# Optimization experiments

Hardware: AMD Instinct MI355X
Metric: run time of the kernel (lower is better)

The kernel has to match this reference:

```python
import jax, jax.numpy as jnp
import numpy as np

EPS = 1e-6
NUM_HEADS = 16


def _layernorm(x, g, b):
    m = jnp.mean(x, axis=-1, keepdims=True)
    v = jnp.mean(jnp.square(x - m), axis=-1, keepdims=True)
    return (x - m) / jnp.sqrt(v + EPS) * g + b


def _rotate_half(x):
    x1, x2 = jnp.split(x, 2, axis=-1)
    return jnp.concatenate([-x2, x1], axis=-1)


def setup_inputs() -> dict:
    key = jax.random.key(0)
    B, N, C = 2, 2048, 1024
    H = NUM_HEADS
    D = C // H
    F = int(C * 4.0)
    ks = jax.random.split(key, 12)
    s = 0.02
    pos = jnp.arange(N)[:, None].astype(jnp.float32)
    inv_freq = 1.0 / (10000.0 ** (jnp.arange(0, D, 2, dtype=jnp.float32) / D))
    freqs = pos * inv_freq[None, :]          # [N, D/2]
    emb = jnp.concatenate([freqs, freqs], axis=-1)  # [N, D]
    return {
        "x": jax.random.normal(ks[0], (B, N, C), jnp.float32),
        "rotary_cos": jnp.cos(emb),
        "rotary_sin": jnp.sin(emb),
        "ln1_g": jnp.ones((C,), jnp.float32),
        "ln1_b": jnp.zeros((C,), jnp.float32),
        "Wq": jax.random.normal(ks[1], (C, C), jnp.float32) * s,
        "bq": jnp.zeros((C,), jnp.float32),
        "Wk": jax.random.normal(ks[2], (C, C), jnp.float32) * s,
        "bk": jnp.zeros((C,), jnp.float32),
        "Wv": jax.random.normal(ks[3], (C, C), jnp.float32) * s,
        "bv": jnp.zeros((C,), jnp.float32),
        "Wo": jax.random.normal(ks[4], (C, C), jnp.float32) * s,
        "bo": jnp.zeros((C,), jnp.float32),
        "ln2_g": jnp.ones((C,), jnp.float32),
        "ln2_b": jnp.zeros((C,), jnp.float32),
        "W1": jax.random.normal(ks[5], (F, C), jnp.float32) * s,
        "b1": jnp.zeros((F,), jnp.float32),
        "W2": jax.random.normal(ks[6], (C, F), jnp.float32) * s,
        "b2": jnp.zeros((C,), jnp.float32),
    }


def reference(x, rotary_cos, rotary_sin, ln1_g, ln1_b, Wq, bq, Wk, bk, Wv, bv,
              Wo, bo, ln2_g, ln2_b, W1, b1, W2, b2):
    B, N, C = x.shape
    H = NUM_HEADS
    D = C // H

    # --- attention branch ---
    h = _layernorm(x, ln1_g, ln1_b)
    q = (h @ Wq.T + bq).reshape(B, N, H, D).transpose(0, 2, 1, 3)  # [B,H,N,D]
    k = (h @ Wk.T + bk).reshape(B, N, H, D).transpose(0, 2, 1, 3)
    v = (h @ Wv.T + bv).reshape(B, N, H, D).transpose(0, 2, 1, 3)

    cos = rotary_cos[None, None, :, :]  # [1,1,N,D]
    sin = rotary_sin[None, None, :, :]
    q = q * cos + _rotate_half(q) * sin
    k = k * cos + _rotate_half(k) * sin

    scale = D ** -0.5
    attn = jnp.einsum('bhnd,bhmd->bhnm', q, k) * scale
    attn = jax.nn.softmax(attn, axis=-1)
    out = jnp.einsum('bhnm,bhmd->bhnd', attn, v)
    out = out.transpose(0, 2, 1, 3).reshape(B, N, C)
    out = out @ Wo.T + bo
    x = x + out

    # --- MLP branch ---
    h = _layernorm(x, ln2_g, ln2_b)
    h = jax.nn.gelu(h @ W1.T + b1, approximate=False)  # torch nn.GELU exact
    h = h @ W2.T + b2
    return x + h
```

## Files before the change

kernel.cpp:

```cpp
#include <hip/hip_runtime.h>
#include <hip/hip_bf16.h>

#define B_ 2
#define N_ 2048
#define C_ 1024
#define H_ 16
#define D_ 64
#define F_ 4096
#define M_ 4096

typedef __attribute__((ext_vector_type(8))) short bf16x8;
typedef __attribute__((ext_vector_type(4))) float f32x4;

__device__ inline unsigned short f2bf(float f) {
  unsigned int u = __float_as_uint(f);
  u = (u + 0x7FFFu + ((u >> 16) & 1u)) >> 16;
  return (unsigned short)u;
}
__device__ inline float bf2f(unsigned short u) {
  unsigned int x = ((unsigned int)u) << 16;
  return __uint_as_float(x);
}

__global__ __launch_bounds__(256)
void cvt_all(const float4* __restrict__ s0, const float4* __restrict__ s1,
             const float4* __restrict__ s2, const float4* __restrict__ s3,
             const float4* __restrict__ s4, const float4* __restrict__ s5,
             ushort4* __restrict__ d0, ushort4* __restrict__ d1,
             ushort4* __restrict__ d2, ushort4* __restrict__ d3,
             ushort4* __restrict__ d4, ushort4* __restrict__ d5) {
  int b = blockIdx.x;
  const float4* s; ushort4* d; int i;
  if      (b < 1024) { s = s0; d = d0; i = b * 256 + threadIdx.x; }
  else if (b < 2048) { s = s1; d = d1; i = (b - 1024) * 256 + threadIdx.x; }
  else if (b < 3072) { s = s2; d = d2; i = (b - 2048) * 256 + threadIdx.x; }
  else if (b < 4096) { s = s3; d = d3; i = (b - 3072) * 256 + threadIdx.x; }
  else if (b < 8192) { s = s4; d = d4; i = (b - 4096) * 256 + threadIdx.x; }
  else               { s = s5; d = d5; i = (b - 8192) * 256 + threadIdx.x; }
  float4 f = s[i];
  ushort4 o;
  o.x = f2bf(f.x); o.y = f2bf(f.y); o.z = f2bf(f.z); o.w = f2bf(f.w);
  d[i] = o;
}

__global__ __launch_bounds__(256)
void ln_kernel(const float* __restrict__ x, const float* __restrict__ g,
               const float* __restrict__ b, unsigned short* __restrict__ out) {
  __shared__ float red[8];
  const int row = blockIdx.x;
  const int t = threadIdx.x;
  const float4 xv = *(const float4*)(x + row * 1024 + t * 4);
  float s  = xv.x + xv.y + xv.z + xv.w;
  float sq = xv.x * xv.x + xv.y * xv.y + xv.z * xv.z + xv.w * xv.w;
  #pragma unroll
  for (int off = 32; off >= 1; off >>= 1) {
    s  += __shfl_down(s, off);
    sq += __shfl_down(sq, off);
  }
  const int lane = t & 63, wave = t >> 6;
  if (lane == 0) { red[wave * 2] = s; red[wave * 2 + 1] = sq; }
  __syncthreads();
  float ts = red[0] + red[2] + red[4] + red[6];
  float tq = red[1] + red[3] + red[5] + red[7];
  float mean = ts * (1.0f / 1024.0f);
  float var  = tq * (1.0f / 1024.0f) - mean * mean;
  float rstd = rsqrtf(var + 1e-6f);
  float xs[4] = {xv.x, xv.y, xv.z, xv.w};
  #pragma unroll
  for (int i = 0; i < 4; i++) {
    int c = t * 4 + i;
    float y = (xs[i] - mean) * rstd * g[c] + b[c];
    out[row * 1024 + c] = f2bf(y);
  }
}

template<int MODE, int BN>
__global__ __launch_bounds__(256)
void gemm_bt(const unsigned short* __restrict__ A,
             const unsigned short* __restrict__ Bw,
             int K, int Nout, int npc,
             const float* __restrict__ bias,
             const float* __restrict__ resid,
             unsigned short* __restrict__ out_bf,
             float* __restrict__ out_f32) {
  constexpr int NJ = BN / 32;
  static_assert(BN == 64, "vmcnt literal assumes 6 loads per stage");
  __shared__ unsigned short sA[3][128 * 64];
  __shared__ unsigned short sB[3][BN * 64];
  const int t = threadIdx.x;
  const int wave = t >> 6, lane = t & 63;
  const int quad = lane >> 4, l16 = lane & 15;
  const int wm = (wave & 1) * 64, wn = (wave >> 1) * (BN / 2);
  const int id = blockIdx.y * gridDim.x + blockIdx.x;
  const int xcd = id & 7, r_ = id >> 3;
  const int m_blk = xcd * 4 + (r_ & 3);
  const int n_blk = r_ >> 2;
  const int m0 = m_blk * 128, n0 = n_blk * BN;

  f32x4 acc[4][NJ];
  #pragma unroll
  for (int i = 0; i < 4; i++)
    #pragma unroll
    for (int j = 0; j < NJ; j++) acc[i][j] = (f32x4){0.f, 0.f, 0.f, 0.f};

  const int sc = (((t & 7) ^ ((t >> 3) & 7)) * 8);
  const unsigned short* gA = A  + (m0 + (t >> 3)) * K + sc;
  const unsigned short* gB = Bw + (n0 + (t >> 3)) * K + sc;

  auto stage = [&](int k0, int buf) {
    unsigned short* lA = &sA[buf][(wave * 8) * 64];
    unsigned short* lB = &sB[buf][(wave * 8) * 64];
    #pragma unroll
    for (int i = 0; i < 4; i++)
      __builtin_amdgcn_global_load_lds((const unsigned int*)(gA + (32 * i) * K + k0),
                                       (unsigned int*)(lA + 32 * i * 64), 16, 0, 0);
    #pragma unroll
    for (int i = 0; i < BN / 32; i++)
      __builtin_amdgcn_global_load_lds((const unsigned int*)(gB + (32 * i) * K + k0),
                                       (unsigned int*)(lB + 32 * i * 64), 16, 0, 0);
  };

  stage(0, 0);
  stage(64, 1);
  asm volatile("s_waitcnt vmcnt(6)" ::: "memory");
  __builtin_amdgcn_s_barrier();

  const int so0 = ((quad ^ (l16 & 7)) * 8);
  const int so1 = (((4 + quad) ^ (l16 & 7)) * 8);

  const int nk = K >> 6;
  int cur = 0;
  for (int kt = 0; kt < nk; kt++) {
    const unsigned short* rA = &sA[cur][0];
    const unsigned short* rB = &sB[cur][0];
    #pragma unroll
    for (int kk = 0; kk < 2; kk++) {
      const int so = kk ? so1 : so0;
      bf16x8 af[4], bfr[NJ];
      #pragma unroll
      for (int i = 0; i < 4; i++)
        af[i] = *(const bf16x8*)(&rA[(wm + i * 16 + l16) * 64 + so]);
      #pragma unroll
      for (int j = 0; j < NJ; j++)
        bfr[j] = *(const bf16x8*)(&rB[(wn + j * 16 + l16) * 64 + so]);
      #pragma unroll
      for (int i = 0; i < 4; i++)
        #pragma unroll
        for (int j = 0; j < NJ; j++)
          acc[i][j] = __builtin_amdgcn_mfma_f32_16x16x32_bf16(af[i], bfr[j], acc[i][j], 0, 0, 0);
    }
    if (kt + 2 < nk) {
      const int nb = (cur + 2 >= 3) ? cur - 1 : cur + 2;
      stage((kt + 2) * 64, nb);
      asm volatile("s_waitcnt vmcnt(6)" ::: "memory");
    } else {
      asm volatile("s_waitcnt vmcnt(0)" ::: "memory");
    }
    __builtin_amdgcn_s_barrier();
    cur = (cur == 2) ? 0 : cur + 1;
  }

  #pragma unroll
  for (int i = 0; i < 4; i++) {
    #pragma unroll
    for (int j = 0; j < NJ; j++) {
      int col = n0 + wn + j * 16 + l16;
      #pragma unroll
      for (int r = 0; r < 4; r++) {
        int row = m0 + wm + i * 16 + quad * 4 + r;
        float v = acc[i][j][r];
        if (MODE == 1 || MODE == 3) {
          out_f32[row * Nout + col] = v + bias[col] + resid[row * Nout + col];
        } else {
          v += bias[col];
          float w = v * (1.0f + 0.044715f * v * v);
          float gl = v / (1.0f + __expf(-1.5957691216f * w));
          out_bf[row * Nout + col] = f2bf(gl);
        }
      }
    }
  }
}

template<int EPI>
__global__ __launch_bounds__(512, 1)
void gemm256(const unsigned short* __restrict__ A,
             const unsigned short* __restrict__ Bw,
             const float* __restrict__ bias,
             const float* __restrict__ bq, const float* __restrict__ bk,
             const float* __restrict__ bv,
             const float* __restrict__ rc, const float* __restrict__ rs,
             unsigned short* __restrict__ o0,
             unsigned short* __restrict__ ko, unsigned short* __restrict__ vt) {
  const int K = 1024;
  __shared__ unsigned short sA[2][256 * 64];
  __shared__ unsigned short sB[2][256 * 64];
  const int t = threadIdx.x;
  const int wave = t >> 6, lane = t & 63;
  const int quad = lane >> 4, l16 = lane & 15;
  const int wm = (wave & 1) * 128, wn = (wave >> 1) * 64;
  const int id = blockIdx.x;
  const int xcd = id & 7, r_ = id >> 3;
  int m_blk, n_blk;
  if (EPI == 0) { n_blk = xcd * 2 + (r_ >> 4); m_blk = r_ & 15; }
  else          { m_blk = xcd * 2 + r_ / 12;   n_blk = r_ % 12; }
  const int m0 = m_blk * 256, n0 = n_blk * 256;

  f32x4 acc[8][4];
  #pragma unroll
  for (int i = 0; i < 8; i++)
    #pragma unroll
    for (int j = 0; j < 4; j++) acc[i][j] = (f32x4){0.f, 0.f, 0.f, 0.f};

  const int sc = (((t & 7) ^ ((t >> 3) & 7)) * 8);
  const unsigned short* gA = A  + (m0 + (t >> 3)) * K + sc;
  const unsigned short* gB = Bw + (n0 + (t >> 3)) * K + sc;

  auto stage_pair = [&](int k0, int buf, int pr) {
    if (pr < 2) {
      unsigned short* lA = &sA[buf][(wave * 8) * 64];
      #pragma unroll
      for (int r = pr * 2; r < pr * 2 + 2; r++)
        __builtin_amdgcn_global_load_lds((const unsigned int*)(gA + (64 * r) * K + k0),
                                         (unsigned int*)(lA + 64 * r * 64), 16, 0, 0);
    } else {
      unsigned short* lB = &sB[buf][(wave * 8) * 64];
      #pragma unroll
      for (int r = (pr - 2) * 2; r < (pr - 2) * 2 + 2; r++)
        __builtin_amdgcn_global_load_lds((const unsigned int*)(gB + (64 * r) * K + k0),
                                         (unsigned int*)(lB + 64 * r * 64), 16, 0, 0);
    }
  };

  stage_pair(0, 0, 0); stage_pair(0, 0, 1); stage_pair(0, 0, 2); stage_pair(0, 0, 3);
  stage_pair(64, 1, 0);
  asm volatile("s_waitcnt vmcnt(2)" ::: "memory");
  __builtin_amdgcn_s_barrier();

  const int so0 = ((quad ^ (l16 & 7)) * 8);
  const int so1 = (((4 + quad) ^ (l16 & 7)) * 8);

  const int nk = K >> 6;
  for (int t_ = 0; t_ < nk; t_++) {
    const int R = t_ & 1;
    const unsigned short* rA = sA[R];
    const unsigned short* rB = sB[R];
    #pragma unroll
    for (int kk = 0; kk < 2; kk++) {
      const int so = kk ? so1 : so0;
      bf16x8 af[8], bfr[4];
      #pragma unroll
      for (int ii = 0; ii < 8; ii++)
        af[ii] = *(const bf16x8*)(&rA[(wm + ii * 16 + l16) * 64 + so]);
      #pragma unroll
      for (int j = 0; j < 4; j++)
        bfr[j] = *(const bf16x8*)(&rB[(wn + j * 16 + l16) * 64 + so]);
      if (t_ + 1 < nk) {
        if (kk == 0) {
          stage_pair((t_ + 1) * 64, R ^ 1, 1);
        } else {
          stage_pair((t_ + 1) * 64, R ^ 1, 2);
          stage_pair((t_ + 1) * 64, R ^ 1, 3);
        }
      }
      __builtin_amdgcn_s_barrier();
      asm volatile("s_waitcnt lgkmcnt(0)" ::: "memory");
      __builtin_amdgcn_sched_barrier(0);
      __builtin_amdgcn_s_setprio(1);
      #pragma unroll
      for (int ii = 0; ii < 8; ii++)
        #pragma unroll
        for (int j = 0; j < 4; j++)
          acc[ii][j] =
              __builtin_amdgcn_mfma_f32_16x16x32_bf16(af[ii], bfr[j], acc[ii][j], 0, 0, 0);
      __builtin_amdgcn_s_setprio(0);
      if (kk == 0) __builtin_amdgcn_s_barrier();
    }
    __builtin_amdgcn_s_barrier();
    if (t_ + 2 < nk) {
      stage_pair((t_ + 2) * 64, R, 0);
      asm volatile("s_waitcnt vmcnt(2)" ::: "memory");
      __builtin_amdgcn_s_barrier();
    } else if (t_ + 1 < nk) {
      asm volatile("s_waitcnt vmcnt(0)" ::: "memory");
      __builtin_amdgcn_s_barrier();
    }
  }

  if (EPI == 0) {
    #pragma unroll
    for (int i = 0; i < 8; i++) {
      #pragma unroll
      for (int j = 0; j < 4; j++) {
        int col = n0 + wn + j * 16 + l16;
        float bb = bias[col];
        #pragma unroll
        for (int r = 0; r < 4; r++) {
          int row = m0 + wm + i * 16 + quad * 4 + r;
          float v = acc[i][j][r] + bb;
          float w = v * (1.0f + 0.044715f * v * v);
          float gl = v / (1.0f + __expf(-1.5957691216f * w));
          o0[row * 4096 + col] = f2bf(gl);
        }
      }
    }
  } else {
    const int rgn = n_blk >> 2;
    const int c0 = (n_blk & 3) * 256;
    if (rgn == 2) {
      #pragma unroll
      for (int i = 0; i < 8; i++) {
        int row0 = m0 + wm + i * 16 + quad * 4;
        int bidx = row0 >> 11, n0r = row0 & 2047;
        #pragma unroll
        for (int j = 0; j < 4; j++) {
          int d = j * 16 + l16;
          int c = c0 + wn + d;
          int h = c >> 6;
          float bb = bv[c];
          __hip_bfloat162 p01 = __float22bfloat162_rn(float2{acc[i][j][0] + bb, acc[i][j][1] + bb});
          __hip_bfloat162 p23 = __float22bfloat162_rn(float2{acc[i][j][2] + bb, acc[i][j][3] + bb});
          unsigned int u01, u23;
          __builtin_memcpy(&u01, &p01, 4);
          __builtin_memcpy(&u23, &p23, 4);
          *(uint2*)(vt + (((bidx * 16 + h) * 64) + d) * 2048 + n0r) = make_uint2(u01, u23);
        }
      }
    } else {
      const float* bia = (rgn == 0) ? bq : bk;
      unsigned short* outp = (rgn == 0) ? o0 : ko;
      #pragma unroll
      for (int i = 0; i < 8; i++) {
        #pragma unroll
        for (int r = 0; r < 4; r++) {
          int row = m0 + wm + i * 16 + quad * 4 + r;
          int bidx = row >> 11, n = row & 2047;
          #pragma unroll
          for (int j = 0; j < 4; j++) {
            int d = j * 16 + l16;
            int c = c0 + wn + d;
            int h = c >> 6;
            int oi = ((bidx * 16 + h) * 2048 + n) * 64 + d;
            float val = acc[i][j][r] + bia[c];
            float pv  = acc[i][j ^ 2][r] + bia[c ^ 32];
            float rot = (j < 2) ? -pv : pv;
            float y = val * rc[n * 64 + d] + rot * rs[n * 64 + d];
            if (rgn == 0) y *= 0.125f;
            outp[oi] = f2bf(y);
          }
        }
      }
    }
  }
}

__global__ __launch_bounds__(512)
void flash_attn(const unsigned short* __restrict__ q,
                const unsigned short* __restrict__ k,
                const unsigned short* __restrict__ vt,
                unsigned short* __restrict__ o0h,
                unsigned short* __restrict__ o1h,
                float* __restrict__ l0g, float* __restrict__ l1g) {
  __shared__ unsigned short sK[2][64 * 64];
  __shared__ unsigned short sVt[2][64 * 64];
  __shared__ unsigned short sPt[2][8][16 * 72];
  const int t = threadIdx.x;
  const int wave = t >> 6, lane = t & 63;
  const int quad = lane >> 4, l16 = lane & 15;
  const int id = blockIdx.x;
  const int bh = (id & 7) * 4 + ((id >> 3) & 3);
  const int qb = (id >> 5) & 7;
  const int kvh = id >> 8;
  const int base = bh * (N_ * D_);

  bf16x8 qa[2][2];
  #pragma unroll
  for (int qt = 0; qt < 2; qt++) {
    int qrow = qb * 256 + wave * 32 + qt * 16 + l16;
    #pragma unroll
    for (int kk = 0; kk < 2; kk++)
      qa[qt][kk] = *(const bf16x8*)(q + base + qrow * D_ + kk * 32 + quad * 8);
  }
  float l_i[2] = {0.f, 0.f};
  f32x4 o_acc[2][4];
  #pragma unroll
  for (int qt = 0; qt < 2; qt++)
    #pragma unroll
    for (int dt = 0; dt < 4; dt++) o_acc[qt][dt] = (f32x4){0.f, 0.f, 0.f, 0.f};

  const int sc = (((t & 7) ^ ((t >> 3) & 7)) * 8);
  const unsigned short* gK  = k  + base + (t >> 3) * 64 + sc;
  const unsigned short* gVt = vt + bh * (64 * 2048) + (t >> 3) * 2048 + sc;

  auto stage = [&](int kt, int buf) {
    __builtin_amdgcn_global_load_lds((const unsigned int*)(gK + kt * 64 * 64),
                                     (unsigned int*)(&sK[buf][(wave * 8) * 64]), 16, 0, 0);
    __builtin_amdgcn_global_load_lds((const unsigned int*)(gVt + kt * 64),
                                     (unsigned int*)(&sVt[buf][(wave * 8) * 64]), 16, 0, 0);
  };
  const int kt0 = kvh * 16, kt1 = kt0 + 16;
  stage(kt0, 0);
  __syncthreads();

  const int so0 = ((quad ^ (l16 & 7)) * 8);
  const int so1 = (((4 + quad) ^ (l16 & 7)) * 8);

  for (int kt = kt0; kt < kt1; kt++) {
    const int cur = kt & 1;
    if (kt + 1 < kt1) stage(kt + 1, cur ^ 1);

    f32x4 s_acc[2][4];
    #pragma unroll
    for (int nt = 0; nt < 4; nt++) {
      bf16x8 kb0 = *(const bf16x8*)(&sK[cur][(nt * 16 + l16) * 64 + so0]);
      bf16x8 kb1 = *(const bf16x8*)(&sK[cur][(nt * 16 + l16) * 64 + so1]);
      #pragma unroll
      for (int qt = 0; qt < 2; qt++) {
        f32x4 a = (f32x4){0.f, 0.f, 0.f, 0.f};
        a = __builtin_amdgcn_mfma_f32_16x16x32_bf16(kb0, qa[qt][0], a, 0, 0, 0);
        a = __builtin_amdgcn_mfma_f32_16x16x32_bf16(kb1, qa[qt][1], a, 0, 0, 0);
        s_acc[qt][nt] = a;
      }
    }
    #pragma unroll
    for (int qt = 0; qt < 2; qt++) {
      float rsum = 0.f;
      #pragma unroll
      for (int nt = 0; nt < 4; nt++)
        #pragma unroll
        for (int r = 0; r < 4; r++) {
          float p = __expf(s_acc[qt][nt][r]);
          s_acc[qt][nt][r] = p;
          rsum += p;
        }
      rsum += __shfl_xor(rsum, 16);
      rsum += __shfl_xor(rsum, 32);
      l_i[qt] += rsum;
      #pragma unroll
      for (int nt = 0; nt < 4; nt++) {
        __hip_bfloat162 p01 = __float22bfloat162_rn(float2{s_acc[qt][nt][0], s_acc[qt][nt][1]});
        __hip_bfloat162 p23 = __float22bfloat162_rn(float2{s_acc[qt][nt][2], s_acc[qt][nt][3]});
        unsigned int u01, u23;
        __builtin_memcpy(&u01, &p01, 4);
        __builtin_memcpy(&u23, &p23, 4);
        *(uint2*)(&sPt[qt][wave][l16 * 72 + nt * 16 + quad * 4]) = make_uint2(u01, u23);
      }
    }
    __asm__ volatile("s_waitcnt lgkmcnt(0)" ::: "memory");
    bf16x8 pt[2][2];
    #pragma unroll
    for (int qt = 0; qt < 2; qt++) {
      pt[qt][0] = *(const bf16x8*)(&sPt[qt][wave][l16 * 72 + quad * 8]);
      pt[qt][1] = *(const bf16x8*)(&sPt[qt][wave][l16 * 72 + 32 + quad * 8]);
    }
    #pragma unroll
    for (int dt = 0; dt < 4; dt++) {
      int d0 = dt * 16 + l16;
      bf16x8 va0 = *(const bf16x8*)(&sVt[cur][d0 * 64 + so0]);
      bf16x8 va1 = *(const bf16x8*)(&sVt[cur][d0 * 64 + so1]);
      #pragma unroll
      for (int qt = 0; qt < 2; qt++) {
        o_acc[qt][dt] = __builtin_amdgcn_mfma_f32_16x16x32_bf16(va0, pt[qt][0], o_acc[qt][dt], 0, 0, 0);
        o_acc[qt][dt] = __builtin_amdgcn_mfma_f32_16x16x32_bf16(va1, pt[qt][1], o_acc[qt][dt], 0, 0, 0);
      }
    }
    __syncthreads();
  }

  unsigned short* op = kvh ? o1h : o0h;
  float* lp = kvh ? l1g : l0g;
  const int b = bh >> 4, h = bh & 15;
  #pragma unroll
  for (int qt = 0; qt < 2; qt++) {
    const int qrow = qb * 256 + wave * 32 + qt * 16 + l16;
    if (quad == 0) lp[bh * 2048 + qrow] = l_i[qt];
    const int tok = b * N_ + qrow;
    #pragma unroll
    for (int dt = 0; dt < 4; dt++) {
      __hip_bfloat162 p01 = __float22bfloat162_rn(float2{o_acc[qt][dt][0], o_acc[qt][dt][1]});
      __hip_bfloat162 p23 = __float22bfloat162_rn(float2{o_acc[qt][dt][2], o_acc[qt][dt][3]});
      unsigned int u01, u23;
      __builtin_memcpy(&u01, &p01, 4);
      __builtin_memcpy(&u23, &p23, 4);
      int col = h * 64 + dt * 16 + quad * 4;
      *(uint2*)(op + tok * C_ + col) = make_uint2(u01, u23);
    }
  }
}

__global__ __launch_bounds__(256)
void attn_norm(const unsigned short* __restrict__ o0h,
               const unsigned short* __restrict__ o1h,
               const float* __restrict__ l0g, const float* __restrict__ l1g,
               unsigned short* __restrict__ o) {
  const int i = (blockIdx.x * 256 + threadIdx.x) * 8;
  const int row = i >> 10, c = i & 1023;
  const int h = c >> 6;
  const int b = row >> 11, n = row & 2047;
  const int li = (b * 16 + h) * 2048 + n;
  const float inv = 1.0f / (l0g[li] + l1g[li]);
  ushort4 a0 = *(const ushort4*)(o0h + i);
  ushort4 a1 = *(const ushort4*)(o0h + i + 4);
  ushort4 b0 = *(const ushort4*)(o1h + i);
  ushort4 b1 = *(const ushort4*)(o1h + i + 4);
  ushort4 r0, r1;
  r0.x = f2bf((bf2f(a0.x) + bf2f(b0.x)) * inv);
  r0.y = f2bf((bf2f(a0.y) + bf2f(b0.y)) * inv);
  r0.z = f2bf((bf2f(a0.z) + bf2f(b0.z)) * inv);
  r0.w = f2bf((bf2f(a0.w) + bf2f(b0.w)) * inv);
  r1.x = f2bf((bf2f(a1.x) + bf2f(b1.x)) * inv);
  r1.y = f2bf((bf2f(a1.y) + bf2f(b1.y)) * inv);
  r1.z = f2bf((bf2f(a1.z) + bf2f(b1.z)) * inv);
  r1.w = f2bf((bf2f(a1.w) + bf2f(b1.w)) * inv);
  *(ushort4*)(o + i) = r0;
  *(ushort4*)(o + i + 4) = r1;
}

extern "C" void kernel_launch(void* const* d_in, const int* in_sizes, int n_in,
                              void* d_out, int out_size, void* d_ws, size_t ws_size,
                              hipStream_t stream) {
  const float* x   = (const float*)d_in[0];
  const float* rc  = (const float*)d_in[1];
  const float* rs  = (const float*)d_in[2];
  const float* g1  = (const float*)d_in[3];
  const float* be1 = (const float*)d_in[4];
  const float* Wq  = (const float*)d_in[5];
  const float* bq  = (const float*)d_in[6];
  const float* Wk  = (const float*)d_in[7];
  const float* bk  = (const float*)d_in[8];
  const float* Wv  = (const float*)d_in[9];
  const float* bv  = (const float*)d_in[10];
  const float* Wo  = (const float*)d_in[11];
  const float* bo  = (const float*)d_in[12];
  const float* g2  = (const float*)d_in[13];
  const float* be2 = (const float*)d_in[14];
  const float* W1  = (const float*)d_in[15];
  const float* b1m = (const float*)d_in[16];
  const float* W2  = (const float*)d_in[17];
  const float* b2m = (const float*)d_in[18];
  float* out = (float*)d_out;

  char* ws = (char*)d_ws;
  unsigned short* wqkv = (unsigned short*)(ws + 0);
  unsigned short* wo   = (unsigned short*)(ws + 6291456);
  unsigned short* w1   = (unsigned short*)(ws + 8388608);
  unsigned short* w2   = (unsigned short*)(ws + 16777216);
  unsigned short* h1   = (unsigned short*)(ws + 25165824);
  unsigned short* qa   = (unsigned short*)(ws + 33554432);
  unsigned short* ka   = (unsigned short*)(ws + 41943040);
  unsigned short* va   = (unsigned short*)(ws + 50331648);
  unsigned short* ao   = (unsigned short*)(ws + 58720256);
  float*          x1   = (float*)(ws + 67108864);
  float*          l0   = (float*)(ws + 67108864);
  float*          l1   = l0 + 65536;
  unsigned short* u    = (unsigned short*)(ws + 33554432);

  cvt_all<<<12288, 256, 0, stream>>>(
      (const float4*)Wq, (const float4*)Wk, (const float4*)Wv, (const float4*)Wo,
      (const float4*)W1, (const float4*)W2,
      (ushort4*)wqkv, (ushort4*)(wqkv + 1048576), (ushort4*)(wqkv + 2097152),
      (ushort4*)wo, (ushort4*)w1, (ushort4*)w2);

  ln_kernel<<<4096, 256, 0, stream>>>(x, g1, be1, h1);
  gemm256<1><<<192, 512, 0, stream>>>(h1, wqkv, nullptr, bq, bk, bv, rc, rs, qa, ka, va);
  flash_attn<<<512, 512, 0, stream>>>(qa, ka, va, ao, h1, l0, l1);
  attn_norm<<<2048, 256, 0, stream>>>(ao, h1, l0, l1, ao);
  gemm_bt<1, 64><<<dim3(16, 32), 256, 0, stream>>>(ao, wo, 1024, 1024, 2, bo, x, nullptr, x1);
  ln_kernel<<<4096, 256, 0, stream>>>(x1, g2, be2, h1);
  gemm256<0><<<256, 512, 0, stream>>>(h1, w1, b1m, nullptr, nullptr, nullptr, nullptr, nullptr,
                                      u, nullptr, nullptr);
  gemm_bt<3, 64><<<dim3(16, 32), 256, 0, stream>>>(u, w2, 4096, 1024, 2, b2m, x1, nullptr, out);
}
```

Before: 364.1 us.

## Replace 256x256 GEMM with smaller-tile QKV kernel and reuse gemm_bt for FC1

Removes the large 256x256-tile, 512-thread gemm256 kernel. The QKV projection now uses a new 128x64-tile, 256-thread kernel with a three-stage LDS ring buffer and one head per N-tile, which simplifies the RoPE and V-transpose epilogue. FC1 with GELU switches to the existing gemm_bt<2,64> kernel. Smaller tiles launch many more blocks to improve occupancy and load balance, at the cost of less data reuse per tile and more global traffic.

Result: no change. 360.4 us (-1.0%).

```diff
diff --git a/kernel.cpp b/kernel.cpp
--- a/kernel.cpp
+++ b/kernel.cpp
@@ -182,33 +182,30 @@
   }
 }
 
-template<int EPI>
-__global__ __launch_bounds__(512, 1)
-void gemm256(const unsigned short* __restrict__ A,
-             const unsigned short* __restrict__ Bw,
-             const float* __restrict__ bias,
-             const float* __restrict__ bq, const float* __restrict__ bk,
-             const float* __restrict__ bv,
-             const float* __restrict__ rc, const float* __restrict__ rs,
-             unsigned short* __restrict__ o0,
-             unsigned short* __restrict__ ko, unsigned short* __restrict__ vt) {
-  const int K = 1024;
-  __shared__ unsigned short sA[2][256 * 64];
-  __shared__ unsigned short sB[2][256 * 64];
+__global__ __launch_bounds__(256)
+void gemm_qkv_t4(const unsigned short* __restrict__ A,
+                 const unsigned short* __restrict__ Bw,
+                 const float* __restrict__ bq, const float* __restrict__ bk,
+                 const float* __restrict__ bv,
+                 const float* __restrict__ rc, const float* __restrict__ rs,
+                 unsigned short* __restrict__ qo, unsigned short* __restrict__ ko,
+                 unsigned short* __restrict__ vt) {
+  const int K = C_;
+  __shared__ unsigned short sA[3][128 * 64];
+  __shared__ unsigned short sB[3][64 * 64];
   const int t = threadIdx.x;
   const int wave = t >> 6, lane = t & 63;
   const int quad = lane >> 4, l16 = lane & 15;
-  const int wm = (wave & 1) * 128, wn = (wave >> 1) * 64;
+  const int wm = wave * 32;
   const int id = blockIdx.x;
   const int xcd = id & 7, r_ = id >> 3;
-  int m_blk, n_blk;
-  if (EPI == 0) { n_blk = xcd * 2 + (r_ >> 4); m_blk = r_ & 15; }
-  else          { m_blk = xcd * 2 + r_ / 12;   n_blk = r_ % 12; }
-  const int m0 = m_blk * 256, n0 = n_blk * 256;
-
-  f32x4 acc[8][4];
-  #pragma unroll
-  for (int i = 0; i < 8; i++)
+  const int m_blk = xcd * 4 + (r_ & 3);
+  const int n_blk = r_ >> 2;
+  const int m0 = m_blk * 128, n0 = n_blk * 64;
+
+  f32x4 acc[2][4];
+  #pragma unroll
+  for (int i = 0; i < 2; i++)
     #pragma unroll
     for (int j = 0; j < 4; j++) acc[i][j] = (f32x4){0.f, 0.f, 0.f, 0.f};
 
@@ -216,138 +213,99 @@
   const unsigned short* gA = A  + (m0 + (t >> 3)) * K + sc;
   const unsigned short* gB = Bw + (n0 + (t >> 3)) * K + sc;
 
-  auto stage_pair = [&](int k0, int buf, int pr) {
-    if (pr < 2) {
-      unsigned short* lA = &sA[buf][(wave * 8) * 64];
-      #pragma unroll
-      for (int r = pr * 2; r < pr * 2 + 2; r++)
-        __builtin_amdgcn_global_load_lds((const unsigned int*)(gA + (64 * r) * K + k0),
-                                         (unsigned int*)(lA + 64 * r * 64), 16, 0, 0);
-    } else {
-      unsigned short* lB = &sB[buf][(wave * 8) * 64];
-      #pragma unroll
-      for (int r = (pr - 2) * 2; r < (pr - 2) * 2 + 2; r++)
-        __builtin_amdgcn_global_load_lds((const unsigned int*)(gB + (64 * r) * K + k0),
-                                         (unsigned int*)(lB + 64 * r * 64), 16, 0, 0);
-    }
+  auto stage = [&](int k0, int buf) {
+    unsigned short* lA = &sA[buf][(wave * 8) * 64];
+    unsigned short* lB = &sB[buf][(wave * 8) * 64];
+    #pragma unroll
+    for (int i = 0; i < 4; i++)
+      __builtin_amdgcn_global_load_lds((const unsigned int*)(gA + (32 * i) * K + k0),
+                                       (unsigned int*)(lA + 32 * i * 64), 16, 0, 0);
+    #pragma unroll
+    for (int i = 0; i < 2; i++)
+      __builtin_amdgcn_global_load_lds((const unsigned int*)(gB + (32 * i) * K + k0),
+                                       (unsigned int*)(lB + 32 * i * 64), 16, 0, 0);
   };
 
-  stage_pair(0, 0, 0); stage_pair(0, 0, 1); stage_pair(0, 0, 2); stage_pair(0, 0, 3);
-  stage_pair(64, 1, 0);
-  asm volatile("s_waitcnt vmcnt(2)" ::: "memory");
+  stage(0, 0);
+  stage(64, 1);
+  asm volatile("s_waitcnt vmcnt(6)" ::: "memory");
   __builtin_amdgcn_s_barrier();
 
   const int so0 = ((quad ^ (l16 & 7)) * 8);
   const int so1 = (((4 + quad) ^ (l16 & 7)) * 8);
 
   const int nk = K >> 6;
-  for (int t_ = 0; t_ < nk; t_++) {
-    const int R = t_ & 1;
-    const unsigned short* rA = sA[R];
-    const unsigned short* rB = sB[R];
+  int cur = 0;
+  for (int kt = 0; kt < nk; kt++) {
+    const unsigned short* rA = &sA[cur][0];
+    const unsigned short* rB = &sB[cur][0];
     #pragma unroll
     for (int kk = 0; kk < 2; kk++) {
       const int so = kk ? so1 : so0;
-      bf16x8 af[8], bfr[4];
-      #pragma unroll
-      for (int ii = 0; ii < 8; ii++)
-        af[ii] = *(const bf16x8*)(&rA[(wm + ii * 16 + l16) * 64 + so]);
+      bf16x8 af[2], bfr[4];
+      #pragma unroll
+      for (int i = 0; i < 2; i++)
+        af[i] = *(const bf16x8*)(&rA[(wm + i * 16 + l16) * 64 + so]);
       #pragma unroll
       for (int j = 0; j < 4; j++)
-        bfr[j] = *(const bf16x8*)(&rB[(wn + j * 16 + l16) * 64 + so]);
-      if (t_ + 1 < nk) {
-        if (kk == 0) {
-          stage_pair((t_ + 1) * 64, R ^ 1, 1);
-        } else {
-          stage_pair((t_ + 1) * 64, R ^ 1, 2);
-          stage_pair((t_ + 1) * 64, R ^ 1, 3);
-        }
-      }
-      __builtin_amdgcn_s_barrier();
-      asm volatile("s_waitcnt lgkmcnt(0)" ::: "memory");
-      __builtin_amdgcn_sched_barrier(0);
-      __builtin_amdgcn_s_setprio(1);
-      #pragma unroll
-      for (int ii = 0; ii < 8; ii++)
+        bfr[j] = *(const bf16x8*)(&rB[(j * 16 + l16) * 64 + so]);
+      #pragma unroll
+      for (int i = 0; i < 2; i++)
         #pragma unroll
         for (int j = 0; j < 4; j++)
-          acc[ii][j] =
-              __builtin_amdgcn_mfma_f32_16x16x32_bf16(af[ii], bfr[j], acc[ii][j], 0, 0, 0);
-      __builtin_amdgcn_s_setprio(0);
-      if (kk == 0) __builtin_amdgcn_s_barrier();
+          acc[i][j] = __builtin_amdgcn_mfma_f32_16x16x32_bf16(af[i], bfr[j], acc[i][j], 0, 0, 0);
+    }
+    if (kt + 2 < nk) {
+      const int nb = (cur + 2 >= 3) ? cur - 1 : cur + 2;
+      stage((kt + 2) * 64, nb);
+      asm volatile("s_waitcnt vmcnt(6)" ::: "memory");
+    } else {
+      asm volatile("s_waitcnt vmcnt(0)" ::: "memory");
     }
     __builtin_amdgcn_s_barrier();
-    if (t_ + 2 < nk) {
-      stage_pair((t_ + 2) * 64, R, 0);
-      asm volatile("s_waitcnt vmcnt(2)" ::: "memory");
-      __builtin_amdgcn_s_barrier();
-    } else if (t_ + 1 < nk) {
-      asm volatile("s_waitcnt vmcnt(0)" ::: "memory");
-      __builtin_amdgcn_s_barrier();
-    }
-  }
-
-  if (EPI == 0) {
-    #pragma unroll
-    for (int i = 0; i < 8; i++) {
+    cur = (cur == 2) ? 0 : cur + 1;
+  }
+
+  const int rgn = n_blk >> 4;
+  const int h   = n_blk & 15;
+
+  if (rgn == 2) {
+    #pragma unroll
+    for (int i = 0; i < 2; i++) {
+      int row0 = m0 + wm + i * 16 + quad * 4;
+      int bidx = row0 >> 11, n0r = row0 & 2047;
       #pragma unroll
       for (int j = 0; j < 4; j++) {
-        int col = n0 + wn + j * 16 + l16;
-        float bb = bias[col];
-        #pragma unroll
-        for (int r = 0; r < 4; r++) {
-          int row = m0 + wm + i * 16 + quad * 4 + r;
-          float v = acc[i][j][r] + bb;
-          float w = v * (1.0f + 0.044715f * v * v);
-          float gl = v / (1.0f + __expf(-1.5957691216f * w));
-          o0[row * 4096 + col] = f2bf(gl);
-        }
+        int d = j * 16 + l16;
+        float bb = bv[h * 64 + d];
+        __hip_bfloat162 p01 = __float22bfloat162_rn(float2{acc[i][j][0] + bb, acc[i][j][1] + bb});
+        __hip_bfloat162 p23 = __float22bfloat162_rn(float2{acc[i][j][2] + bb, acc[i][j][3] + bb});
+        unsigned int u01, u23;
+        __builtin_memcpy(&u01, &p01, 4);
+        __builtin_memcpy(&u23, &p23, 4);
+        *(uint2*)(vt + (((bidx * 16 + h) * 64) + d) * 2048 + n0r) = make_uint2(u01, u23);
       }
     }
   } else {
-    const int rgn = n_blk >> 2;
-    const int c0 = (n_blk & 3) * 256;
-    if (rgn == 2) {
-      #pragma unroll
-      for (int i = 0; i < 8; i++) {
-        int row0 = m0 + wm + i * 16 + quad * 4;
-        int bidx = row0 >> 11, n0r = row0 & 2047;
+    const float* bia = (rgn == 0) ? bq : bk;
+    unsigned short* outp = (rgn == 0) ? qo : ko;
+    #pragma unroll
+    for (int i = 0; i < 2; i++) {
+      #pragma unroll
+      for (int r = 0; r < 4; r++) {
+        int row = m0 + wm + i * 16 + quad * 4 + r;
+        int bidx = row >> 11, n = row & 2047;
         #pragma unroll
         for (int j = 0; j < 4; j++) {
           int d = j * 16 + l16;
-          int c = c0 + wn + d;
-          int h = c >> 6;
-          float bb = bv[c];
-          __hip_bfloat162 p01 = __float22bfloat162_rn(float2{acc[i][j][0] + bb, acc[i][j][1] + bb});
-          __hip_bfloat162 p23 = __float22bfloat162_rn(float2{acc[i][j][2] + bb, acc[i][j][3] + bb});
-          unsigned int u01, u23;
-          __builtin_memcpy(&u01, &p01, 4);
-          __builtin_memcpy(&u23, &p23, 4);
-          *(uint2*)(vt + (((bidx * 16 + h) * 64) + d) * 2048 + n0r) = make_uint2(u01, u23);
-        }
-      }
-    } else {
-      const float* bia = (rgn == 0) ? bq : bk;
-      unsigned short* outp = (rgn == 0) ? o0 : ko;
-      #pragma unroll
-      for (int i = 0; i < 8; i++) {
-        #pragma unroll
-        for (int r = 0; r < 4; r++) {
-          int row = m0 + wm + i * 16 + quad * 4 + r;
-          int bidx = row >> 11, n = row & 2047;
-          #pragma unroll
-          for (int j = 0; j < 4; j++) {
-            int d = j * 16 + l16;
-            int c = c0 + wn + d;
-            int h = c >> 6;
-            int oi = ((bidx * 16 + h) * 2048 + n) * 64 + d;
-            float val = acc[i][j][r] + bia[c];
-            float pv  = acc[i][j ^ 2][r] + bia[c ^ 32];
-            float rot = (j < 2) ? -pv : pv;
-            float y = val * rc[n * 64 + d] + rot * rs[n * 64 + d];
-            if (rgn == 0) y *= 0.125f;
-            outp[oi] = f2bf(y);
-          }
+          int c = h * 64 + d;
+          int oi = ((bidx * 16 + h) * 2048 + n) * 64 + d;
+          float val = acc[i][j][r] + bia[c];
+          float pv  = acc[i][j ^ 2][r] + bia[c ^ 32];
+          float rot = (j < 2) ? -pv : pv;
+          float y = val * rc[n * 64 + d] + rot * rs[n * 64 + d];
+          if (rgn == 0) y *= 0.125f;
+          outp[oi] = f2bf(y);
         }
       }
     }
@@ -562,12 +520,11 @@
       (ushort4*)wo, (ushort4*)w1, (ushort4*)w2);
 
   ln_kernel<<<4096, 256, 0, stream>>>(x, g1, be1, h1);
-  gemm256<1><<<192, 512, 0, stream>>>(h1, wqkv, nullptr, bq, bk, bv, rc, rs, qa, ka, va);
+  gemm_qkv_t4<<<1536, 256, 0, stream>>>(h1, wqkv, bq, bk, bv, rc, rs, qa, ka, va);
   flash_attn<<<512, 512, 0, stream>>>(qa, ka, va, ao, h1, l0, l1);
   attn_norm<<<2048, 256, 0, stream>>>(ao, h1, l0, l1, ao);
   gemm_bt<1, 64><<<dim3(16, 32), 256, 0, stream>>>(ao, wo, 1024, 1024, 2, bo, x, nullptr, x1);
   ln_kernel<<<4096, 256, 0, stream>>>(x1, g2, be2, h1);
-  gemm256<0><<<256, 512, 0, stream>>>(h1, w1, b1m, nullptr, nullptr, nullptr, nullptr, nullptr,
-                                      u, nullptr, nullptr);
+  gemm_bt<2, 64><<<dim3(16, 128), 256, 0, stream>>>(h1, w1, 1024, 4096, 8, b1m, nullptr, u, nullptr);
   gemm_bt<3, 64><<<dim3(16, 32), 256, 0, stream>>>(u, w2, 4096, 1024, 2, b2m, x1, nullptr, out);
 }
```
